# Kernel optimization log

Measured on AMD Instinct MI355X. Metric: run time of the kernel, lower is better.

The kernel has to match this reference:

```python
import jax, jax.numpy as jnp
import numpy as np
from jax import lax

D_MODEL = 192
D_STATE = 128
D_CONV = 3
EXPAND = 2
HEADDIM = 64
NGROUPS = 1
CHUNK = 256
K = 4  # scan directions
D_INNER = EXPAND * D_MODEL          # 384
D_SSM = D_INNER                     # 384
NHEADS = D_SSM // HEADDIM           # 6
HH = K * NHEADS                     # 24 heads total (dir-major)
CONV_CH = D_SSM + 2 * NGROUPS * D_STATE + NHEADS  # 646 (conv applied to x,B,C,dt channels)
D_IN_PROJ = 2 * D_INNER + 2 * NGROUPS * D_STATE + NHEADS  # 1030
BSZ, HIMG, WIMG = 4, 64, 64


def setup_inputs() -> dict:
    key = jax.random.key(0)
    ks = jax.random.split(key, 8)
    u = jax.random.normal(ks[0], (BSZ, HIMG, WIMG, D_MODEL), jnp.float32)
    W_in = jax.random.normal(ks[1], (D_MODEL, D_IN_PROJ), jnp.float32) * 0.02
    conv_w = jax.random.normal(ks[2], (CONV_CH, 1, D_CONV, D_CONV), jnp.float32) * 0.1
    conv_b = jnp.zeros((CONV_CH,), jnp.float32)
    # dt_bias init per source: inverse-softplus of dt ~ LogUniform(1e-3, 1e-1), tiled over 4 dirs
    dt = jnp.exp(jax.random.uniform(ks[3], (NHEADS,)) * (np.log(0.1) - np.log(0.001)) + np.log(0.001))
    dt = jnp.maximum(dt, 1e-4)
    inv_dt = dt + jnp.log(-jnp.expm1(-dt))
    dt_bias = jnp.tile(inv_dt[None, :], (K, 1))  # (4, nheads)
    A = jax.random.uniform(ks[4], (NHEADS,), minval=1.0, maxval=16.0)
    A_logs = jnp.tile(jnp.log(A), (K,))          # (24,)
    Ds = jnp.ones((HH,), jnp.float32)
    norm_w = jnp.ones((D_SSM,), jnp.float32)
    W_out = jax.random.normal(ks[5], (D_INNER, D_MODEL), jnp.float32) * 0.02
    return dict(u=u, W_in=W_in, conv_w=conv_w, conv_b=conv_b, dt_bias=dt_bias,
                A_logs=A_logs, Ds=Ds, norm_w=norm_w, W_out=W_out)


def _ssd(x, dt, A, Bm, Cm, chunk):
    """Chunked selective state-space scan (Mamba2 SSD).
    x: (b,L,H,P), dt: (b,L,H) (post-softplus), A: (H,) negative scalars,
    Bm/Cm: (b,L,G,N) with heads grouped G-major (H = G*hpg)."""
    b, L, H, P = x.shape
    G, N = Bm.shape[2], Bm.shape[3]
    hpg = H // G
    nc = L // chunk
    x = x.reshape(b, nc, chunk, G, hpg, P)
    dt = dt.reshape(b, nc, chunk, G, hpg)
    Bm = Bm.reshape(b, nc, chunk, G, N)
    Cm = Cm.reshape(b, nc, chunk, G, N)
    dA = dt * A.reshape(G, hpg)                 # (b,z,c,g,h), negative
    dAc = jnp.cumsum(dA, axis=2)                # within-chunk cumsum
    dAt = jnp.transpose(dAc, (0, 1, 3, 4, 2))   # (b,z,g,h,c)
    idx = jnp.arange(chunk)
    mask = idx[:, None] >= idx[None, :]         # causal within chunk
    seg = jnp.exp(jnp.where(mask, dAt[..., :, None] - dAt[..., None, :], -1e30))  # (b,z,g,h,c,s)
    CB = jnp.einsum('bzcgn,bzsgn->bzgcs', Cm, Bm)
    xdt = x * dt[..., None]                     # dt applied at source position
    y_intra = jnp.einsum('bzghcs,bzsghp->bzcghp', CB[:, :, :, None] * seg, xdt)
    decay_last = jnp.exp(dAc[:, :, -1:] - dAc)  # (b,z,c,g,h)
    states = jnp.einsum('bzcgn,bzcghp->bzghpn', Bm, xdt * decay_last[..., None])
    cd = jnp.exp(dAc[:, :, -1])                 # (b,z,g,h) whole-chunk decay

    def step(carry, inp):
        s, c = inp
        return carry * c[..., None, None] + s, carry  # emit state entering the chunk

    _, prevs = lax.scan(step, jnp.zeros_like(states[:, 0]),
                        (jnp.swapaxes(states, 0, 1), jnp.swapaxes(cd, 0, 1)))
    prev = jnp.swapaxes(prevs, 0, 1)            # (b,z,g,h,P,N)
    y_inter = jnp.einsum('bzcgn,bzghpn->bzcghp', Cm, prev) * jnp.exp(dAc)[..., None]
    return (y_intra + y_inter).reshape(b, L, H, P)


def reference(u, W_in, conv_w, conv_b, dt_bias, A_logs, Ds, norm_w, W_out):
    B, H, W, C = u.shape
    L = H * W
    zxbcdt = u @ W_in                            # (B,H,W,1030); d_mlp == 0
    z = zxbcdt[..., :D_SSM]                      # gate
    xBCdt = zxbcdt[..., D_SSM:]                  # (B,H,W,CONV_CH)
    # depthwise 3x3 conv + SiLU (NCHW)
    xb = jnp.transpose(xBCdt, (0, 3, 1, 2))
    xb = lax.conv_general_dilated(xb, conv_w, (1, 1), 'SAME',
                                  feature_group_count=CONV_CH,
                                  dimension_numbers=('NCHW', 'OIHW', 'NCHW'))
    xb = jax.nn.silu(xb + conv_b[None, :, None, None])
    # 4 scan directions: row-major, col-major, and their reverses
    d0 = xb.reshape(B, CONV_CH, L)
    d1 = jnp.transpose(xb, (0, 1, 3, 2)).reshape(B, CONV_CH, L)
    dirs = jnp.stack([d0, d1], axis=1)
    dirs = jnp.concatenate([dirs, jnp.flip(dirs, axis=-1)], axis=1)  # (B,4,CONV_CH,L)
    seq = jnp.transpose(dirs, (0, 3, 1, 2))      # (B,L,4,CONV_CH)
    xs = seq[..., :D_SSM].reshape(B, L, HH, HEADDIM)
    Bs = seq[..., D_SSM:D_SSM + D_STATE]         # (B,L,4,N), ngroups=1 -> G=4 dirs
    Cs = seq[..., D_SSM + D_STATE:D_SSM + 2 * D_STATE]
    dts = seq[..., D_SSM + 2 * D_STATE:].reshape(B, L, HH)
    dt = jax.nn.softplus(dts + dt_bias.reshape(HH))
    A = -jnp.exp(A_logs)                         # (HH,)
    y = _ssd(xs, dt, A, Bs, Cs, CHUNK) + xs * Ds[None, None, :, None]
    y = y.reshape(B, L, K, D_SSM)
    y0 = y[:, :, 0]
    y1 = y[:, :, 1]
    y2 = jnp.flip(y[:, :, 2], axis=1)
    y3 = jnp.flip(y[:, :, 3], axis=1)
    wh1 = jnp.transpose(y1.reshape(B, W, H, D_SSM), (0, 2, 1, 3)).reshape(B, L, D_SSM)
    wh3 = jnp.transpose(y3.reshape(B, W, H, D_SSM), (0, 2, 1, 3)).reshape(B, L, D_SSM)
    out = (y0 + y2 + wh1 + wh3).reshape(B, H, W, D_SSM)
    # RMSNormGated (norm_before_gate=False, group_size = d_ssm)
    g = out * jax.nn.silu(z)
    g = g * lax.rsqrt(jnp.mean(g * g, axis=-1, keepdims=True) + 1e-5) * norm_w
    return g @ W_out
```

## Files before the change

kernel.cpp:

```cpp
#include <hip/hip_runtime.h>
#include <hip/hip_fp16.h>
#include <math.h>

#define BQ 4
#define LQ 4096
#define DM 192
#define DIP 1030
#define DSSM 384
#define DST 128
#define CCH 646
#define CH640 640
#define NHD 6
#define KDIR 4
#define NCH 16
#define CLEN 256
#define UH_ELEMS (16384 * 192)
#define WT_ELEMS (1152 * 192)

using half8 = __attribute__((ext_vector_type(8))) _Float16;
using half4 = __attribute__((ext_vector_type(4))) _Float16;
using f32x4 = __attribute__((ext_vector_type(4))) float;

#define XWI(pp, ss) ((pp) * 72 + ((((ss) >> 3) ^ ((pp) >> 3)) << 3) + ((ss) & 7))
#define XW2(n, ss) ((n) * 72 + (((((ss) >> 3) ^ ((n) >> 3)) & 7) << 3) + ((ss) & 7))

__device__ __forceinline__ int pixof(int k, int t) {
  switch (k) {
    case 0: return t;
    case 1: return ((t & 63) << 6) | (t >> 6);
    case 2: return 4095 - t;
    default: { int tp = 4095 - t; return ((tp & 63) << 6) | (tp >> 6); }
  }
}

__device__ __forceinline__ float softplusf(float x) {
  return (x > 20.f) ? x : log1pf(expf(x));
}
__device__ __forceinline__ float siluf(float x) {
  return x / (1.f + __expf(-x));
}

__global__ void k_cvt(const float* __restrict__ u, const float* __restrict__ W,
                      _Float16* __restrict__ uh, _Float16* __restrict__ whT) {
  int idx = blockIdx.x * 256 + threadIdx.x;
  if (idx < UH_ELEMS) uh[idx] = (_Float16)u[idx];
  int widx = idx - UH_ELEMS;
  if (widx >= 0 && widx < WT_ELEMS) {
    int n = widx / 192, kk = widx - n * 192;
    whT[widx] = (n < DIP) ? (_Float16)W[(size_t)kk * DIP + n] : (_Float16)0.f;
  }
}

__global__ __launch_bounds__(256) void k_inproj(
    const _Float16* __restrict__ uh, const _Float16* __restrict__ whT,
    __half* __restrict__ zh, __half* __restrict__ xbch, float* __restrict__ xdt32) {
  __shared__ __align__(16) _Float16 sA[128 * 72];
  __shared__ __align__(16) _Float16 sB[128 * 72];
  int nt = blockIdx.x, mt = blockIdx.y;
  int m0 = mt * 128, n0 = nt * 128;
  int t = threadIdx.x, lane = t & 63, w = t >> 6;
  int acol = lane & 15, koff = (lane >> 4) * 8;
  int wr = w >> 1, wc = w & 1;
  f32x4 zz = {0.f, 0.f, 0.f, 0.f};
  f32x4 acc[4][4];
#pragma unroll
  for (int fr = 0; fr < 4; ++fr)
#pragma unroll
    for (int fc = 0; fc < 4; ++fc) acc[fr][fc] = zz;
  for (int kk = 0; kk < 3; ++kk) {
    if (kk) __syncthreads();
#pragma unroll
    for (int i = 0; i < 4; ++i) {
      int task = t + i * 256;
      int row = task >> 3, oct = task & 7;
      *(half8*)&sA[row * 72 + oct * 8] =
          *(const half8*)&uh[(size_t)(m0 + row) * 192 + kk * 64 + oct * 8];
      *(half8*)&sB[row * 72 + oct * 8] =
          *(const half8*)&whT[(size_t)(n0 + row) * 192 + kk * 64 + oct * 8];
    }
    __syncthreads();
#pragma unroll
    for (int ks = 0; ks < 2; ++ks) {
      half8 af[4], bf[4];
#pragma unroll
      for (int f = 0; f < 4; ++f) {
        af[f] = *(const half8*)&sA[(wr * 64 + f * 16 + acol) * 72 + ks * 32 + koff];
        bf[f] = *(const half8*)&sB[(wc * 64 + f * 16 + acol) * 72 + ks * 32 + koff];
      }
#pragma unroll
      for (int fr = 0; fr < 4; ++fr)
#pragma unroll
        for (int fc = 0; fc < 4; ++fc)
          acc[fr][fc] = __builtin_amdgcn_mfma_f32_16x16x32_f16(af[fr], bf[fc], acc[fr][fc], 0, 0, 0);
    }
  }
  int rb = (lane >> 4) * 4;
#pragma unroll
  for (int fr = 0; fr < 4; ++fr) {
#pragma unroll
    for (int fc = 0; fc < 4; ++fc) {
      int n = n0 + wc * 64 + fc * 16 + acol;
#pragma unroll
      for (int r = 0; r < 4; ++r) {
        int m = m0 + wr * 64 + fr * 16 + rb + r;
        float v = acc[fr][fc][r];
        if (n < DSSM) zh[(size_t)m * DSSM + n] = (__half)v;
        else if (n < 1024) xbch[(size_t)m * CH640 + (n - DSSM)] = (__half)v;
        else if (n < DIP) xdt32[(size_t)m * NHD + (n - 1024)] = v;
      }
    }
  }
}

__global__ void k_conv(const __half* __restrict__ xbch, const float* __restrict__ xdt,
                       const float* __restrict__ cw, const float* __restrict__ cb,
                       __half* __restrict__ convh, float* __restrict__ dtraw) {
  int pid = blockIdx.x;
  int b = pid >> 12, p = pid & 4095;
  int y = p >> 6, x = p & 63;
  int t = threadIdx.x;
  const __half2* baseh2 = (const __half2*)(xbch + (size_t)b * LQ * CH640);
  __half2* outh2 = (__half2*)(convh + (size_t)pid * CH640);
  for (int pc = t; pc < 320; pc += 256) {
    int c0 = pc * 2;
    float s0 = 0.f, s1 = 0.f;
#pragma unroll
    for (int ky = 0; ky < 3; ++ky) {
      int yy = y + ky - 1;
      if (yy < 0 || yy > 63) continue;
#pragma unroll
      for (int kx = 0; kx < 3; ++kx) {
        int xx = x + kx - 1;
        if (xx < 0 || xx > 63) continue;
        __half2 v = baseh2[(size_t)(yy * 64 + xx) * 320 + pc];
        int wi = ky * 3 + kx;
        s0 += (float)v.x * cw[c0 * 9 + wi];
        s1 += (float)v.y * cw[(c0 + 1) * 9 + wi];
      }
    }
    __half2 o;
    o.x = (__half)siluf(s0 + cb[c0]);
    o.y = (__half)siluf(s1 + cb[c0 + 1]);
    outh2[pc] = o;
  }
  if (t < NHD) {
    const float* based = xdt + (size_t)b * LQ * NHD;
    float s = 0.f;
#pragma unroll
    for (int ky = 0; ky < 3; ++ky) {
      int yy = y + ky - 1;
      if (yy < 0 || yy > 63) continue;
#pragma unroll
      for (int kx = 0; kx < 3; ++kx) {
        int xx = x + kx - 1;
        if (xx < 0 || xx > 63) continue;
        s += based[(size_t)(yy * 64 + xx) * NHD + t] * cw[(CH640 + t) * 9 + ky * 3 + kx];
      }
    }
    dtraw[(size_t)pid * NHD + t] = siluf(s + cb[CH640 + t]);
  }
}

__global__ void k_prep(const float* __restrict__ dtraw, const float* __restrict__ dt_bias,
                       const float* __restrict__ A_logs,
                       float* __restrict__ dtb, float* __restrict__ dacb) {
  __shared__ float sb[CLEN];
  int z = blockIdx.x, k = blockIdx.y, b = blockIdx.z;
  int s = threadIdx.x;
  int pixel = pixof(k, z * CLEN + s);
  const float* row = dtraw + ((size_t)(b * LQ + pixel)) * NHD;
  float raw[NHD];
#pragma unroll
  for (int h = 0; h < NHD; ++h) raw[h] = row[h];
  size_t base = (((size_t)(b * KDIR + k) * NCH + z) * NHD) * CLEN;
  for (int h = 0; h < NHD; ++h) {
    float dtv = softplusf(raw[h] + dt_bias[k * NHD + h]);
    float dA = dtv * (-expf(A_logs[k * NHD + h]));
    sb[s] = dA;
    __syncthreads();
    for (int off = 1; off < CLEN; off <<= 1) {
      float v = (s >= off) ? sb[s - off] : 0.f;
      __syncthreads();
      sb[s] += v;
      __syncthreads();
    }
    dtb[base + (size_t)h * CLEN + s] = dtv;
    dacb[base + (size_t)h * CLEN + s] = sb[s];
    __syncthreads();
  }
}

__global__ __launch_bounds__(256, 4) void k_cb(const _Float16* __restrict__ convh,
                                               _Float16* __restrict__ cbuf) {
  __shared__ __align__(16) char smem[34816];
  _Float16* sCt = (_Float16*)smem;
  _Float16* sBt = (_Float16*)(smem + 17408);
  int pi = blockIdx.x, z = blockIdx.y, bk = blockIdx.z;
  int b = bk >> 2, kd = bk & 3;
  int SI = 0;
  while ((SI + 1) * (SI + 2) / 2 <= pi) ++SI;
  int SJ = pi - SI * (SI + 1) / 2;
  int t = threadIdx.x, lane = t & 63, w = t >> 6;
  int acol = lane & 15, koff = (lane >> 4) * 8;
  int R = w * 16, arow = R + acol, rbase = R + (lane >> 4) * 4;
  const _Float16* convb = convh + (size_t)b * LQ * CH640;
  for (int i = 0; i < 4; ++i) {
    int c = t + i * 256;
    int row = c >> 4, seg = c & 15;
    int pc = pixof(kd, z * CLEN + SI * 64 + row);
    *(half8*)&sCt[row * 136 + seg * 8] =
        *(const half8*)&convb[(size_t)pc * CH640 + (DSSM + DST) + seg * 8];
    int pbx = pixof(kd, z * CLEN + SJ * 64 + row);
    *(half8*)&sBt[row * 136 + seg * 8] =
        *(const half8*)&convb[(size_t)pbx * CH640 + DSSM + seg * 8];
  }
  __syncthreads();
  f32x4 zz = {0.f, 0.f, 0.f, 0.f};
  f32x4 acc[4] = {zz, zz, zz, zz};
  for (int ks = 0; ks < 4; ++ks) {
    half8 a = *(const half8*)&sCt[arow * 136 + ks * 32 + koff];
#pragma unroll
    for (int cg = 0; cg < 4; ++cg) {
      half8 bf = *(const half8*)&sBt[(cg * 16 + acol) * 136 + ks * 32 + koff];
      acc[cg] = __builtin_amdgcn_mfma_f32_16x16x32_f16(a, bf, acc[cg], 0, 0, 0);
    }
  }
  size_t base = ((size_t)(bk * NCH + z) * 10 + pi) * 4096;
#pragma unroll
  for (int cg = 0; cg < 4; ++cg)
#pragma unroll
    for (int r = 0; r < 4; ++r)
      cbuf[base + (size_t)(rbase + r) * 64 + cg * 16 + acol] = (_Float16)acc[cg][r];
}

__global__ __launch_bounds__(256, 4) void k_states(
    const _Float16* __restrict__ convh, const float* __restrict__ dtb,
    const float* __restrict__ dacb, _Float16* __restrict__ statesT) {
  __shared__ __align__(16) _Float16 sA[64 * 72];
  __shared__ __align__(16) _Float16 sB2[128 * 72];
  __shared__ float sFac[CLEN];
  int h = blockIdx.x, z = blockIdx.y, bk = blockIdx.z;
  int b = bk >> 2, kd = bk & 3;
  int t = threadIdx.x, lane = t & 63, w = t >> 6;
  int acol = lane & 15, koct = lane >> 4;
  size_t dbase = (((size_t)bk * NCH + z) * NHD + h) * CLEN;
  {
    float dac_last = dacb[dbase + CLEN - 1];
    sFac[t] = dtb[dbase + t] * __expf(dac_last - dacb[dbase + t]);
  }
  __syncthreads();
  const _Float16* convb = convh + (size_t)b * LQ * CH640;
  f32x4 zz = {0.f, 0.f, 0.f, 0.f};
  f32x4 acc[8] = {zz, zz, zz, zz, zz, zz, zz, zz};
  for (int st = 0; st < 4; ++st) {
    if (st) __syncthreads();
#pragma unroll
    for (int i = 0; i < 2; ++i) {
      int c = t + i * 256;
      int ss = c >> 3, pp0 = (c & 7) * 8;
      int sg = st * 64 + ss;
      int px = pixof(kd, z * CLEN + sg);
      half8 xv = *(const half8*)&convb[(size_t)px * CH640 + h * 64 + pp0];
      float f = sFac[sg];
#pragma unroll
      for (int u = 0; u < 8; ++u) sA[XWI(pp0 + u, ss)] = (_Float16)((float)xv[u] * f);
    }
#pragma unroll
    for (int i = 0; i < 4; ++i) {
      int c = t + i * 256;
      int ss = c >> 4, n0 = (c & 15) * 8;
      int sg = st * 64 + ss;
      int px = pixof(kd, z * CLEN + sg);
      half8 bv = *(const half8*)&convb[(size_t)px * CH640 + DSSM + n0];
#pragma unroll
      for (int u = 0; u < 8; ++u) sB2[XW2(n0 + u, ss)] = bv[u];
    }
    __syncthreads();
#pragma unroll
    for (int ks = 0; ks < 2; ++ks) {
      int kso = ks * 4 + koct;
      int arow = w * 16 + acol;
      half8 a = *(const half8*)&sA[arow * 72 + ((kso ^ (arow >> 3)) << 3)];
#pragma unroll
      for (int nf = 0; nf < 8; ++nf) {
        int col = nf * 16 + acol;
        half8 bf = *(const half8*)&sB2[col * 72 + (((kso ^ (col >> 3)) & 7) << 3)];
        acc[nf] = __builtin_amdgcn_mfma_f32_16x16x32_f16(a, bf, acc[nf], 0, 0, 0);
      }
    }
  }
  size_t sbase = (((size_t)bk * NCH + z) * NHD + h) * (128 * 64);
  int rbase = koct * 4;
#pragma unroll
  for (int nf = 0; nf < 8; ++nf) {
    int col = nf * 16 + acol;
#pragma unroll
    for (int r = 0; r < 4; ++r)
      statesT[sbase + (size_t)(w * 16 + rbase + r) * 128 + col] = (_Float16)acc[nf][r];
  }
}

__global__ void k_scan(_Float16* __restrict__ states, const float* __restrict__ dacb) {
  int h = blockIdx.x, k = blockIdx.y, b = blockIdx.z;
  int bk = b * KDIR + k;
  int t = threadIdx.x;
  float carry[32];
#pragma unroll
  for (int j = 0; j < 32; ++j) carry[j] = 0.f;
  for (int z = 0; z < NCH; ++z) {
    float cd = __expf(dacb[(((size_t)bk * NCH + z) * NHD + h) * CLEN + (CLEN - 1)]);
    size_t sbase = (((size_t)bk * NCH + z) * NHD + h) * (128 * 64);
#pragma unroll
    for (int j = 0; j < 32; ++j) {
      size_t idx = sbase + (size_t)j * 256 + t;
      float sv = (float)states[idx];
      states[idx] = (_Float16)carry[j];
      carry[j] = carry[j] * cd + sv;
    }
  }
}

__global__ __launch_bounds__(256, 4) void k_y(
    const _Float16* __restrict__ convh, const float* __restrict__ dtb,
    const float* __restrict__ dacb, const _Float16* __restrict__ cbuf,
    const _Float16* __restrict__ prevT, const float* __restrict__ Ds,
    _Float16* __restrict__ ybuf) {
  __shared__ __align__(16) _Float16 sPrev[64 * 136];
  __shared__ __align__(16) _Float16 sXW[64 * 72];
  __shared__ __align__(16) _Float16 sA[64 * 72];
  __shared__ float sdt[CLEN], sdac[CLEN], sFac[CLEN];
  __shared__ float sExpD[64], sRs[64];

  int wg = blockIdx.x;
  int xid = (wg & 7) * 192 + (wg >> 3);
  int h = xid % 6;
  int bkz = xid / 6;
  int bk = bkz >> 4, z = bkz & 15;
  int b = bk >> 2, kd = bk & 3;
  int t = threadIdx.x, lane = t & 63, w = t >> 6;
  int acol = lane & 15, koff = (lane >> 4) * 8;
  int R = w * 16, arow = R + acol, rbase = R + (lane >> 4) * 4;

  size_t dbase = (((size_t)bk * NCH + z) * NHD + h) * CLEN;
  sdt[t] = dtb[dbase + t];
  sdac[t] = dacb[dbase + t];
  const _Float16* pbp = prevT + (((size_t)bk * NCH + z) * NHD + h) * (128 * 64);
#pragma unroll
  for (int i = 0; i < 4; ++i) {
    int idx = t + i * 256;
    int p = idx >> 4, seg = idx & 15;
    *(half8*)&sPrev[p * 136 + seg * 8] = *(const half8*)&pbp[(size_t)p * 128 + seg * 8];
  }
  __syncthreads();
  const _Float16* convb = convh + (size_t)b * LQ * CH640;
  float dsv = Ds[kd * NHD + h];
  f32x4 zz = {0.f, 0.f, 0.f, 0.f};

  for (int si_t = 0; si_t < 4; ++si_t) {
    float ref = sdac[si_t * 64];
    sFac[t] = __expf(ref - sdac[t]);
    if (t < 64) {
      float d = sdac[si_t * 64 + t];
      sExpD[t] = __expf(d);
      sRs[t] = __expf(d - ref);
    }
    __syncthreads();
    float eD[4], rsv[4];
#pragma unroll
    for (int r = 0; r < 4; ++r) { eD[r] = sExpD[rbase + r]; rsv[r] = sRs[rbase + r]; }
    f32x4 accE[4] = {zz, zz, zz, zz};
    f32x4 accI[4] = {zz, zz, zz, zz};
    int pxa = pixof(kd, z * CLEN + si_t * 64 + arow);
#pragma unroll
    for (int ks = 0; ks < 4; ++ks) {
      half8 a = *(const half8*)&convb[(size_t)pxa * CH640 + (DSSM + DST) + ks * 32 + koff];
#pragma unroll
      for (int cg = 0; cg < 4; ++cg) {
        half8 bf = *(const half8*)&sPrev[(cg * 16 + acol) * 136 + ks * 32 + koff];
        accE[cg] = __builtin_amdgcn_mfma_f32_16x16x32_f16(a, bf, accE[cg], 0, 0, 0);
      }
    }
    for (int SJ = 0; SJ < si_t; ++SJ) {
#pragma unroll
      for (int i = 0; i < 2; ++i) {
        int c = t + i * 256;
        int ss = c >> 3, pp0 = (c & 7) * 8;
        int sg = SJ * 64 + ss;
        int px = pixof(kd, z * CLEN + sg);
        half8 xv = *(const half8*)&convb[(size_t)px * CH640 + h * 64 + pp0];
        float f = sdt[sg] * sFac[sg];
#pragma unroll
        for (int u = 0; u < 8; ++u)
          sXW[XWI(pp0 + u, ss)] = (_Float16)((float)xv[u] * f);
      }
      __syncthreads();
      size_t cbase = ((size_t)(bk * NCH + z) * 10 + si_t * (si_t + 1) / 2 + SJ) * 4096;
#pragma unroll
      for (int ks = 0; ks < 2; ++ks) {
        half8 a = *(const half8*)&cbuf[cbase + (size_t)arow * 64 + ks * 32 + koff];
        int kso = ks * 4 + (lane >> 4);
#pragma unroll
        for (int cg = 0; cg < 4; ++cg) {
          int col = cg * 16 + acol;
          half8 bf = *(const half8*)&sXW[col * 72 + ((kso ^ (col >> 3)) << 3)];
          accI[cg] = __builtin_amdgcn_mfma_f32_16x16x32_f16(a, bf, accI[cg], 0, 0, 0);
        }
      }
      __syncthreads();
    }
#pragma unroll
    for (int cg = 0; cg < 4; ++cg)
#pragma unroll
      for (int r = 0; r < 4; ++r) accI[cg][r] *= rsv[r];
    {
      size_t cbase = ((size_t)(bk * NCH + z) * 10 + si_t * (si_t + 1) / 2 + si_t) * 4096;
#pragma unroll
      for (int i = 0; i < 16; ++i) {
        int e = t + i * 256;
        int sl = e >> 6, ss = e & 63;
        float cv = 0.f;
        if (ss <= sl)
          cv = (float)cbuf[cbase + e] * __expf(sdac[si_t * 64 + sl] - sdac[si_t * 64 + ss]);
        sA[sl * 72 + ss] = (_Float16)cv;
      }
#pragma unroll
      for (int i = 0; i < 2; ++i) {
        int c = t + i * 256;
        int ss = c >> 3, pp0 = (c & 7) * 8;
        int sg = si_t * 64 + ss;
        int px = pixof(kd, z * CLEN + sg);
        half8 xv = *(const half8*)&convb[(size_t)px * CH640 + h * 64 + pp0];
        float f = sdt[sg];
#pragma unroll
        for (int u = 0; u < 8; ++u)
          sXW[XWI(pp0 + u, ss)] = (_Float16)((float)xv[u] * f);
      }
      __syncthreads();
#pragma unroll
      for (int ks = 0; ks < 2; ++ks) {
        half8 a = *(const half8*)&sA[arow * 72 + ks * 32 + koff];
        int kso = ks * 4 + (lane >> 4);
#pragma unroll
        for (int cg = 0; cg < 4; ++cg) {
          int col = cg * 16 + acol;
          half8 bf = *(const half8*)&sXW[col * 72 + ((kso ^ (col >> 3)) << 3)];
          accI[cg] = __builtin_amdgcn_mfma_f32_16x16x32_f16(a, bf, accI[cg], 0, 0, 0);
        }
      }
    }
#pragma unroll
    for (int cg = 0; cg < 4; ++cg) {
      int col = cg * 16 + acol;
#pragma unroll
      for (int r = 0; r < 4; ++r) {
        int row = rbase + r;
        int tg = z * CLEN + si_t * 64 + row;
        int px = pixof(kd, tg);
        float xv = (float)convb[(size_t)px * CH640 + h * 64 + col];
        float yv = accI[cg][r] + eD[r] * accE[cg][r] + dsv * xv;
        ybuf[((size_t)bk * LQ + tg) * DSSM + h * 64 + col] = (_Float16)yv;
      }
    }
  }
}

__global__ void k_final(const __half* __restrict__ yb, const __half* __restrict__ zh,
                        const float* __restrict__ norm_w, const float* __restrict__ Wout,
                        float* __restrict__ out) {
  __shared__ float sg[8 * DSSM];
  __shared__ float srstd[8];
  int m0 = blockIdx.x * 8;
  int t = threadIdx.x;
  for (int rr = 0; rr < 8; ++rr) {
    int m = m0 + rr, b = m >> 12, px = m & 4095;
    int tr = ((px & 63) << 6) | (px >> 6);
    int t0 = px, t1 = tr, t2 = 4095 - px, t3 = 4095 - tr;
    size_t b4 = (size_t)b * 4;
    for (int c = t; c < DSSM; c += 256) {
      float yv = (float)yb[((b4 + 0) * LQ + t0) * DSSM + c] +
                 (float)yb[((b4 + 1) * LQ + t1) * DSSM + c] +
                 (float)yb[((b4 + 2) * LQ + t2) * DSSM + c] +
                 (float)yb[((b4 + 3) * LQ + t3) * DSSM + c];
      float zv = (float)zh[(size_t)m * DSSM + c];
      sg[rr * DSSM + c] = yv * (zv / (1.f + __expf(-zv)));
    }
  }
  __syncthreads();
  {
    int r = t >> 5, j = t & 31;
    float s = 0.f;
    for (int c = j; c < DSSM; c += 32) { float g = sg[r * DSSM + c]; s += g * g; }
    s += __shfl_xor(s, 16, 32);
    s += __shfl_xor(s, 8, 32);
    s += __shfl_xor(s, 4, 32);
    s += __shfl_xor(s, 2, 32);
    s += __shfl_xor(s, 1, 32);
    if (j == 0) srstd[r] = rsqrtf(s / (float)DSSM + 1e-5f);
  }
  __syncthreads();
  for (int rr = 0; rr < 8; ++rr)
    for (int c = t; c < DSSM; c += 256) sg[rr * DSSM + c] *= srstd[rr] * norm_w[c];
  __syncthreads();
  if (t < DM) {
    float a[8];
#pragma unroll
    for (int rr = 0; rr < 8; ++rr) a[rr] = 0.f;
    for (int c = 0; c < DSSM; ++c) {
      float wv = Wout[(size_t)c * DM + t];
#pragma unroll
      for (int rr = 0; rr < 8; ++rr) a[rr] += sg[rr * DSSM + c] * wv;
    }
#pragma unroll
    for (int rr = 0; rr < 8; ++rr) out[(size_t)(m0 + rr) * DM + t] = a[rr];
  }
}

extern "C" void kernel_launch(void* const* d_in, const int* in_sizes, int n_in,
                              void* d_out, int out_size, void* d_ws, size_t ws_size,
                              hipStream_t stream) {
  const float* u = (const float*)d_in[0];
  const float* W_in = (const float*)d_in[1];
  const float* conv_w = (const float*)d_in[2];
  const float* conv_b = (const float*)d_in[3];
  const float* dt_bias = (const float*)d_in[4];
  const float* A_logs = (const float*)d_in[5];
  const float* Ds = (const float*)d_in[6];
  const float* norm_w = (const float*)d_in[7];
  const float* W_out = (const float*)d_in[8];
  float* out = (float*)d_out;

  float* ws = (float*)d_ws;
  size_t off = 0;
  __half* zh = (__half*)(ws + off); off += (size_t)BQ * LQ * DSSM / 2;
  _Float16* uh = (_Float16*)(ws + off); off += (size_t)UH_ELEMS / 2;
  _Float16* whT = (_Float16*)(ws + off); off += (size_t)WT_ELEMS / 2;
  __half* xbch = (__half*)(ws + off); off += (size_t)BQ * LQ * CH640 / 2;
  float* xdt32 = ws + off; off += (size_t)BQ * LQ * NHD;
  __half* convh = (__half*)(ws + off); off += (size_t)BQ * LQ * CH640 / 2;
  float* dtraw = ws + off; off += (size_t)BQ * LQ * NHD;
  float* dtb = ws + off; off += (size_t)BQ * KDIR * NCH * NHD * CLEN;
  float* dacb = ws + off; off += (size_t)BQ * KDIR * NCH * NHD * CLEN;
  _Float16* statesT = (_Float16*)(ws + off); off += (size_t)BQ * KDIR * NCH * NHD * 128 * 64 / 2;
  __half* ybuf = (__half*)(ws + off); off += (size_t)BQ * KDIR * LQ * DSSM / 2;
  _Float16* cbuf = (_Float16*)xbch;

  k_cvt<<<(UH_ELEMS + WT_ELEMS) / 256, 256, 0, stream>>>(u, W_in, uh, whT);
  k_inproj<<<dim3(9, 128), 256, 0, stream>>>(uh, whT, zh, xbch, xdt32);
  k_conv<<<BQ * LQ, 256, 0, stream>>>(xbch, xdt32, conv_w, conv_b, convh, dtraw);
  k_prep<<<dim3(NCH, KDIR, BQ), 256, 0, stream>>>(dtraw, dt_bias, A_logs, dtb, dacb);
  k_cb<<<dim3(10, NCH, BQ * KDIR), 256, 0, stream>>>((const _Float16*)convh, cbuf);
  k_states<<<dim3(NHD, NCH, BQ * KDIR), 256, 0, stream>>>((const _Float16*)convh, dtb, dacb, statesT);
  k_scan<<<dim3(NHD, KDIR, BQ), 256, 0, stream>>>(statesT, dacb);
  k_y<<<BQ * KDIR * NCH * NHD, 256, 0, stream>>>((const _Float16*)convh, dtb, dacb,
                                                 (const _Float16*)cbuf, statesT, Ds,
                                                 (_Float16*)ybuf);
  k_final<<<BQ * LQ / 8, 256, 0, stream>>>(ybuf, zh, norm_w, W_out, out);
}
```

Before: 491.8 us.

## Split k_y per sub-chunk and precompute decayed diagonal blocks in new kernel

k_y previously looped over four 64-row sub-chunks per workgroup. Each workgroup now handles one sub-chunk, which gives four times as many workgroups and drops the sPrev and sA shared arrays. A new k_diag kernel precomputes the exp-decayed, causally masked diagonal C·B blocks into a global dbuf, which k_y reads directly. Workspace is also rearranged to alias uh/whT with dtraw/dtb/dacb. The trade-off is an extra kernel launch plus dbuf global traffic, and the per-block dtb/dacb loads and exponent setup are now repeated for each sub-chunk.

```diff
diff --git a/kernel.cpp b/kernel.cpp
--- a/kernel.cpp
+++ b/kernel.cpp
@@ -233,6 +233,27 @@
       cbuf[base + (size_t)(rbase + r) * 64 + cg * 16 + acol] = (_Float16)acc[cg][r];
 }
 
+__global__ void k_diag(const _Float16* __restrict__ cbuf, const float* __restrict__ dacb,
+                       _Float16* __restrict__ dbuf) {
+  __shared__ float sd[64];
+  int hs = blockIdx.x;
+  int si = hs / 6, h = hs % 6;
+  int z = blockIdx.y, bk = blockIdx.z;
+  int t = threadIdx.x;
+  if (t < 64) sd[t] = dacb[(((size_t)bk * NCH + z) * NHD + h) * CLEN + si * 64 + t];
+  __syncthreads();
+  size_t cb = ((size_t)(bk * NCH + z) * 10 + si * (si + 1) / 2 + si) * 4096;
+  size_t db = (((size_t)(bk * NCH + z) * 4 + si) * NHD + h) * 4096;
+#pragma unroll
+  for (int i = 0; i < 16; ++i) {
+    int e = t + i * 256;
+    int sl = e >> 6, ss = e & 63;
+    _Float16 v = (_Float16)0.f;
+    if (ss <= sl) v = (_Float16)((float)cbuf[cb + e] * __expf(sd[sl] - sd[ss]));
+    dbuf[db + e] = v;
+  }
+}
+
 __global__ __launch_bounds__(256, 4) void k_states(
     const _Float16* __restrict__ convh, const float* __restrict__ dtb,
     const float* __restrict__ dacb, _Float16* __restrict__ statesT) {
@@ -323,19 +344,17 @@
 __global__ __launch_bounds__(256, 4) void k_y(
     const _Float16* __restrict__ convh, const float* __restrict__ dtb,
     const float* __restrict__ dacb, const _Float16* __restrict__ cbuf,
-    const _Float16* __restrict__ prevT, const float* __restrict__ Ds,
-    _Float16* __restrict__ ybuf) {
-  __shared__ __align__(16) _Float16 sPrev[64 * 136];
+    const _Float16* __restrict__ prevT, const _Float16* __restrict__ dbuf,
+    const float* __restrict__ Ds, _Float16* __restrict__ ybuf) {
   __shared__ __align__(16) _Float16 sXW[64 * 72];
-  __shared__ __align__(16) _Float16 sA[64 * 72];
   __shared__ float sdt[CLEN], sdac[CLEN], sFac[CLEN];
   __shared__ float sExpD[64], sRs[64];
 
   int wg = blockIdx.x;
-  int xid = (wg & 7) * 192 + (wg >> 3);
-  int h = xid % 6;
-  int bkz = xid / 6;
-  int bk = bkz >> 4, z = bkz & 15;
+  int xid = (wg & 7) * 768 + (wg >> 3);
+  int grp = xid / 24, i24 = xid % 24;
+  int h = i24 >> 2, si_t = i24 & 3;
+  int bk = grp >> 4, z = grp & 15;
   int b = bk >> 2, kd = bk & 3;
   int t = threadIdx.x, lane = t & 63, w = t >> 6;
   int acol = lane & 15, koff = (lane >> 4) * 8;
@@ -344,122 +363,109 @@
   size_t dbase = (((size_t)bk * NCH + z) * NHD + h) * CLEN;
   sdt[t] = dtb[dbase + t];
   sdac[t] = dacb[dbase + t];
+  __syncthreads();
+  float ref = sdac[si_t * 64];
+  sFac[t] = __expf(ref - sdac[t]);
+  if (t < 64) {
+    float d = sdac[si_t * 64 + t];
+    sExpD[t] = __expf(d);
+    sRs[t] = __expf(d - ref);
+  }
+  const _Float16* convb = convh + (size_t)b * LQ * CH640;
   const _Float16* pbp = prevT + (((size_t)bk * NCH + z) * NHD + h) * (128 * 64);
-#pragma unroll
-  for (int i = 0; i < 4; ++i) {
-    int idx = t + i * 256;
-    int p = idx >> 4, seg = idx & 15;
-    *(half8*)&sPrev[p * 136 + seg * 8] = *(const half8*)&pbp[(size_t)p * 128 + seg * 8];
-  }
-  __syncthreads();
-  const _Float16* convb = convh + (size_t)b * LQ * CH640;
+  f32x4 zz = {0.f, 0.f, 0.f, 0.f};
+  f32x4 accE[4] = {zz, zz, zz, zz};
+  f32x4 accI[4] = {zz, zz, zz, zz};
+  int pxa = pixof(kd, z * CLEN + si_t * 64 + arow);
+#pragma unroll
+  for (int ks = 0; ks < 4; ++ks) {
+    half8 a = *(const half8*)&convb[(size_t)pxa * CH640 + (DSSM + DST) + ks * 32 + koff];
+#pragma unroll
+    for (int cg = 0; cg < 4; ++cg) {
+      half8 bf = *(const half8*)&pbp[(size_t)(cg * 16 + acol) * 128 + ks * 32 + koff];
+      accE[cg] = __builtin_amdgcn_mfma_f32_16x16x32_f16(a, bf, accE[cg], 0, 0, 0);
+    }
+  }
+  __syncthreads();
+  for (int SJ = 0; SJ < si_t; ++SJ) {
+#pragma unroll
+    for (int i = 0; i < 2; ++i) {
+      int c = t + i * 256;
+      int ss = c >> 3, pp0 = (c & 7) * 8;
+      int sg = SJ * 64 + ss;
+      int px = pixof(kd, z * CLEN + sg);
+      half8 xv = *(const half8*)&convb[(size_t)px * CH640 + h * 64 + pp0];
+      float f = sdt[sg] * sFac[sg];
+#pragma unroll
+      for (int u = 0; u < 8; ++u)
+        sXW[XWI(pp0 + u, ss)] = (_Float16)((float)xv[u] * f);
+    }
+    __syncthreads();
+    size_t cbase = ((size_t)(bk * NCH + z) * 10 + si_t * (si_t + 1) / 2 + SJ) * 4096;
+#pragma unroll
+    for (int ks = 0; ks < 2; ++ks) {
+      half8 a = *(const half8*)&cbuf[cbase + (size_t)arow * 64 + ks * 32 + koff];
+      int kso = ks * 4 + (lane >> 4);
+#pragma unroll
+      for (int cg = 0; cg < 4; ++cg) {
+        int col = cg * 16 + acol;
+        half8 bf = *(const half8*)&sXW[col * 72 + ((kso ^ (col >> 3)) << 3)];
+        accI[cg] = __builtin_amdgcn_mfma_f32_16x16x32_f16(a, bf, accI[cg], 0, 0, 0);
+      }
+    }
+    __syncthreads();
+  }
+  {
+    float rsv[4];
+#pragma unroll
+    for (int r = 0; r < 4; ++r) rsv[r] = sRs[rbase + r];
+#pragma unroll
+    for (int cg = 0; cg < 4; ++cg)
+#pragma unroll
+      for (int r = 0; r < 4; ++r) accI[cg][r] *= rsv[r];
+  }
+  {
+#pragma unroll
+    for (int i = 0; i < 2; ++i) {
+      int c = t + i * 256;
+      int ss = c >> 3, pp0 = (c & 7) * 8;
+      int sg = si_t * 64 + ss;
+      int px = pixof(kd, z * CLEN + sg);
+      half8 xv = *(const half8*)&convb[(size_t)px * CH640 + h * 64 + pp0];
+      float f = sdt[sg];
+#pragma unroll
+      for (int u = 0; u < 8; ++u)
+        sXW[XWI(pp0 + u, ss)] = (_Float16)((float)xv[u] * f);
+    }
+    __syncthreads();
+    size_t db = (((size_t)(bk * NCH + z) * 4 + si_t) * NHD + h) * 4096;
+#pragma unroll
+    for (int ks = 0; ks < 2; ++ks) {
+      half8 a = *(const half8*)&dbuf[db + (size_t)arow * 64 + ks * 32 + koff];
+      int kso = ks * 4 + (lane >> 4);
+#pragma unroll
+      for (int cg = 0; cg < 4; ++cg) {
+        int col = cg * 16 + acol;
+        half8 bf = *(const half8*)&sXW[col * 72 + ((kso ^ (col >> 3)) << 3)];
+        accI[cg] = __builtin_amdgcn_mfma_f32_16x16x32_f16(a, bf, accI[cg], 0, 0, 0);
+      }
+    }
+  }
   float dsv = Ds[kd * NHD + h];
-  f32x4 zz = {0.f, 0.f, 0.f, 0.f};
-
-  for (int si_t = 0; si_t < 4; ++si_t) {
-    float ref = sdac[si_t * 64];
-    sFac[t] = __expf(ref - sdac[t]);
-    if (t < 64) {
-      float d = sdac[si_t * 64 + t];
-      sExpD[t] = __expf(d);
-      sRs[t] = __expf(d - ref);
-    }
-    __syncthreads();
-    float eD[4], rsv[4];
-#pragma unroll
-    for (int r = 0; r < 4; ++r) { eD[r] = sExpD[rbase + r]; rsv[r] = sRs[rbase + r]; }
-    f32x4 accE[4] = {zz, zz, zz, zz};
-    f32x4 accI[4] = {zz, zz, zz, zz};
-    int pxa = pixof(kd, z * CLEN + si_t * 64 + arow);
-#pragma unroll
-    for (int ks = 0; ks < 4; ++ks) {
-      half8 a = *(const half8*)&convb[(size_t)pxa * CH640 + (DSSM + DST) + ks * 32 + koff];
-#pragma unroll
-      for (int cg = 0; cg < 4; ++cg) {
-        half8 bf = *(const half8*)&sPrev[(cg * 16 + acol) * 136 + ks * 32 + koff];
-        accE[cg] = __builtin_amdgcn_mfma_f32_16x16x32_f16(a, bf, accE[cg], 0, 0, 0);
-      }
-    }
-    for (int SJ = 0; SJ < si_t; ++SJ) {
-#pragma unroll
-      for (int i = 0; i < 2; ++i) {
-        int c = t + i * 256;
-        int ss = c >> 3, pp0 = (c & 7) * 8;
-        int sg = SJ * 64 + ss;
-        int px = pixof(kd, z * CLEN + sg);
-        half8 xv = *(const half8*)&convb[(size_t)px * CH640 + h * 64 + pp0];
-        float f = sdt[sg] * sFac[sg];
-#pragma unroll
-        for (int u = 0; u < 8; ++u)
-          sXW[XWI(pp0 + u, ss)] = (_Float16)((float)xv[u] * f);
-      }
-      __syncthreads();
-      size_t cbase = ((size_t)(bk * NCH + z) * 10 + si_t * (si_t + 1) / 2 + SJ) * 4096;
-#pragma unroll
-      for (int ks = 0; ks < 2; ++ks) {
-        half8 a = *(const half8*)&cbuf[cbase + (size_t)arow * 64 + ks * 32 + koff];
-        int kso = ks * 4 + (lane >> 4);
-#pragma unroll
-        for (int cg = 0; cg < 4; ++cg) {
-          int col = cg * 16 + acol;
-          half8 bf = *(const half8*)&sXW[col * 72 + ((kso ^ (col >> 3)) << 3)];
-          accI[cg] = __builtin_amdgcn_mfma_f32_16x16x32_f16(a, bf, accI[cg], 0, 0, 0);
-        }
-      }
-      __syncthreads();
-    }
-#pragma unroll
-    for (int cg = 0; cg < 4; ++cg)
-#pragma unroll
-      for (int r = 0; r < 4; ++r) accI[cg][r] *= rsv[r];
-    {
-      size_t cbase = ((size_t)(bk * NCH + z) * 10 + si_t * (si_t + 1) / 2 + si_t) * 4096;
-#pragma unroll
-      for (int i = 0; i < 16; ++i) {
-        int e = t + i * 256;
-        int sl = e >> 6, ss = e & 63;
-        float cv = 0.f;
-        if (ss <= sl)
-          cv = (float)cbuf[cbase + e] * __expf(sdac[si_t * 64 + sl] - sdac[si_t * 64 + ss]);
-        sA[sl * 72 + ss] = (_Float16)cv;
-      }
-#pragma unroll
-      for (int i = 0; i < 2; ++i) {
-        int c = t + i * 256;
-        int ss = c >> 3, pp0 = (c & 7) * 8;
-        int sg = si_t * 64 + ss;
-        int px = pixof(kd, z * CLEN + sg);
-        half8 xv = *(const half8*)&convb[(size_t)px * CH640 + h * 64 + pp0];
-        float f = sdt[sg];
-#pragma unroll
-        for (int u = 0; u < 8; ++u)
-          sXW[XWI(pp0 + u, ss)] = (_Float16)((float)xv[u] * f);
-      }
-      __syncthreads();
-#pragma unroll
-      for (int ks = 0; ks < 2; ++ks) {
-        half8 a = *(const half8*)&sA[arow * 72 + ks * 32 + koff];
-        int kso = ks * 4 + (lane >> 4);
-#pragma unroll
-        for (int cg = 0; cg < 4; ++cg) {
-          int col = cg * 16 + acol;
-          half8 bf = *(const half8*)&sXW[col * 72 + ((kso ^ (col >> 3)) << 3)];
-          accI[cg] = __builtin_amdgcn_mfma_f32_16x16x32_f16(a, bf, accI[cg], 0, 0, 0);
-        }
-      }
-    }
-#pragma unroll
-    for (int cg = 0; cg < 4; ++cg) {
-      int col = cg * 16 + acol;
-#pragma unroll
-      for (int r = 0; r < 4; ++r) {
-        int row = rbase + r;
-        int tg = z * CLEN + si_t * 64 + row;
-        int px = pixof(kd, tg);
-        float xv = (float)convb[(size_t)px * CH640 + h * 64 + col];
-        float yv = accI[cg][r] + eD[r] * accE[cg][r] + dsv * xv;
-        ybuf[((size_t)bk * LQ + tg) * DSSM + h * 64 + col] = (_Float16)yv;
-      }
+  float eD[4];
+#pragma unroll
+  for (int r = 0; r < 4; ++r) eD[r] = sExpD[rbase + r];
+#pragma unroll
+  for (int cg = 0; cg < 4; ++cg) {
+    int col = cg * 16 + acol;
+#pragma unroll
+    for (int r = 0; r < 4; ++r) {
+      int row = rbase + r;
+      int tg = z * CLEN + si_t * 64 + row;
+      int px = pixof(kd, tg);
+      float xv = (float)convb[(size_t)px * CH640 + h * 64 + col];
+      float yv = accI[cg][r] + eD[r] * accE[cg][r] + dsv * xv;
+      ybuf[((size_t)bk * LQ + tg) * DSSM + h * 64 + col] = (_Float16)yv;
     }
   }
 }
@@ -532,16 +538,18 @@
   float* ws = (float*)d_ws;
   size_t off = 0;
   __half* zh = (__half*)(ws + off); off += (size_t)BQ * LQ * DSSM / 2;
-  _Float16* uh = (_Float16*)(ws + off); off += (size_t)UH_ELEMS / 2;
-  _Float16* whT = (_Float16*)(ws + off); off += (size_t)WT_ELEMS / 2;
+  float* scratch = ws + off; off += 1683456;
+  _Float16* uh = (_Float16*)scratch;
+  _Float16* whT = uh + UH_ELEMS;
+  float* dtraw = scratch;
+  float* dtb = scratch + 98304;
+  float* dacb = scratch + 98304 + 393216;
   __half* xbch = (__half*)(ws + off); off += (size_t)BQ * LQ * CH640 / 2;
   float* xdt32 = ws + off; off += (size_t)BQ * LQ * NHD;
   __half* convh = (__half*)(ws + off); off += (size_t)BQ * LQ * CH640 / 2;
-  float* dtraw = ws + off; off += (size_t)BQ * LQ * NHD;
-  float* dtb = ws + off; off += (size_t)BQ * KDIR * NCH * NHD * CLEN;
-  float* dacb = ws + off; off += (size_t)BQ * KDIR * NCH * NHD * CLEN;
   _Float16* statesT = (_Float16*)(ws + off); off += (size_t)BQ * KDIR * NCH * NHD * 128 * 64 / 2;
   __half* ybuf = (__half*)(ws + off); off += (size_t)BQ * KDIR * LQ * DSSM / 2;
+  _Float16* dbuf = (_Float16*)(ws + off); off += (size_t)BQ * KDIR * NCH * 4 * NHD * 4096 / 2;
   _Float16* cbuf = (_Float16*)xbch;
 
   k_cvt<<<(UH_ELEMS + WT_ELEMS) / 256, 256, 0, stream>>>(u, W_in, uh, whT);
@@ -549,10 +557,11 @@
   k_conv<<<BQ * LQ, 256, 0, stream>>>(xbch, xdt32, conv_w, conv_b, convh, dtraw);
   k_prep<<<dim3(NCH, KDIR, BQ), 256, 0, stream>>>(dtraw, dt_bias, A_logs, dtb, dacb);
   k_cb<<<dim3(10, NCH, BQ * KDIR), 256, 0, stream>>>((const _Float16*)convh, cbuf);
+  k_diag<<<dim3(24, NCH, BQ * KDIR), 256, 0, stream>>>(cbuf, dacb, dbuf);
   k_states<<<dim3(NHD, NCH, BQ * KDIR), 256, 0, stream>>>((const _Float16*)convh, dtb, dacb, statesT);
   k_scan<<<dim3(NHD, KDIR, BQ), 256, 0, stream>>>(statesT, dacb);
-  k_y<<<BQ * KDIR * NCH * NHD, 256, 0, stream>>>((const _Float16*)convh, dtb, dacb,
-                                                 (const _Float16*)cbuf, statesT, Ds,
-                                                 (_Float16*)ybuf);
+  k_y<<<KDIR * NHD * 4 * NCH * BQ, 256, 0, stream>>>((const _Float16*)convh, dtb, dacb,
+                                                     (const _Float16*)cbuf, statesT, dbuf, Ds,
+                                                     (_Float16*)ybuf);
   k_final<<<BQ * LQ / 8, 256, 0, stream>>>(ybuf, zh, norm_w, W_out, out);
 }
```

New measurement: 495.9 us. No clear change (+0.8%).
